# Kernel optimization log

Measured on AMD Instinct MI355X. Metric: run time of the kernel, lower is better.

## Reference

```python
import jax, jax.numpy as jnp
import numpy as np

D = 1024
H = 16
DK = D // H
SCALE = 1.0 / jnp.sqrt(jnp.float32(DK))


def setup_inputs() -> dict:
    key0 = jax.random.key(0)
    ks = jax.random.split(key0, 11)
    B, S = 2, 2048
    std = 1.0 / np.sqrt(D)
    inp = {
        "query": jax.random.normal(ks[0], (B, S, D), jnp.float32),
        "key": jax.random.normal(ks[1], (B, S, D), jnp.float32),
        "value": jax.random.normal(ks[2], (B, S, D), jnp.float32),
        "wq": jax.random.normal(ks[3], (D, D), jnp.float32) * std,
        "bq": jax.random.normal(ks[4], (D,), jnp.float32) * std,
        "wk": jax.random.normal(ks[5], (D, D), jnp.float32) * std,
        "bk": jax.random.normal(ks[6], (D,), jnp.float32) * std,
        "wv": jax.random.normal(ks[7], (D, D), jnp.float32) * std,
        "bv": jax.random.normal(ks[8], (D,), jnp.float32) * std,
        "wo": jax.random.normal(ks[9], (D, D), jnp.float32) * std,
        "bo": jax.random.normal(ks[10], (D,), jnp.float32) * std,
    }
    return inp


def _split_heads(x):
    # [B,S,D] -> [B,H,S,dk]
    B, S, _ = x.shape
    return x.reshape(B, S, H, DK).transpose(0, 2, 1, 3)


def reference(query, key, value, wq, bq, wk, bk, wv, bv, wo, bo):
    B, S, _ = query.shape
    # Linear projections (torch nn.Linear: x @ W^T + b)
    q = _split_heads(query @ wq.T + bq)
    k = _split_heads(key @ wk.T + bk)
    v = _split_heads(value @ wv.T + bv)
    # Scaled dot-product attention scores [B,H,S,S]
    scores = jnp.einsum("bhqd,bhkd->bhqk", q * SCALE, k)
    attention = jax.nn.softmax(scores, axis=-1)
    # Dropout in eval mode == identity
    out = jnp.einsum("bhqk,bhkd->bhqd", attention, v)
    out = out.transpose(0, 2, 1, 3).reshape(B, S, D)
    out = out @ wo.T + bo
    return out, attention
```

## Files before the change

### kernel.cpp

```cpp
#include <hip/hip_runtime.h>
#include <stdint.h>

typedef __attribute__((ext_vector_type(4))) float f32x4;
typedef __attribute__((ext_vector_type(8))) short short8;
typedef __attribute__((ext_vector_type(2))) unsigned int u32x2;

#define MFMA16(a, b, c) __builtin_amdgcn_mfma_f32_16x16x32_bf16((a), (b), (c), 0, 0, 0)

__device__ __forceinline__ unsigned short f2bf(float f) {
  unsigned int x = __float_as_uint(f);
  return (unsigned short)((x + 0x7fffu + ((x >> 16) & 1u)) >> 16);
}

__device__ __forceinline__ unsigned int cvtpk(float lo, float hi) {
  unsigned int d;
  asm("v_cvt_pk_bf16_f32 %0, %1, %2" : "=v"(d) : "v"(lo), "v"(hi));
  return d;
}

__device__ __forceinline__ void gl2lds16(const void* g, void* l) {
  __builtin_amdgcn_global_load_lds((const __attribute__((address_space(1))) void*)g,
                                   (__attribute__((address_space(3))) void*)l, 16, 0, 0);
}

__device__ __forceinline__ void load8cv(const float* __restrict__ s, void* d) {
  const f32x4* p = (const f32x4*)s;
  f32x4 a = p[0], b = p[1];
  short8 t;
  t[0] = (short)f2bf(a[0]); t[1] = (short)f2bf(a[1]);
  t[2] = (short)f2bf(a[2]); t[3] = (short)f2bf(a[3]);
  t[4] = (short)f2bf(b[0]); t[5] = (short)f2bf(b[1]);
  t[6] = (short)f2bf(b[2]); t[7] = (short)f2bf(b[3]);
  *(short8*)d = t;
}

#define BAR_V4 asm volatile("s_waitcnt vmcnt(4)\ns_barrier" ::: "memory")
#define BAR_V0 asm volatile("s_waitcnt vmcnt(0)\ns_barrier" ::: "memory")
#define BAR_RAW asm volatile("s_barrier" ::: "memory")

__global__ __launch_bounds__(256) void cast_weights(const float* __restrict__ wq,
                                                    const float* __restrict__ wk,
                                                    const float* __restrict__ wv,
                                                    const float* __restrict__ wo,
                                                    unsigned short* __restrict__ dst) {
  int i = blockIdx.x * 256 + threadIdx.x;
  int which = i >> 17;
  int off = (i & 131071) * 8;
  const float* src = which == 0 ? wq : which == 1 ? wk : which == 2 ? wv : wo;
  load8cv(src + off, dst + (size_t)which * 1048576 + off);
}

__global__ __launch_bounds__(256) void qkv_proj(const float* __restrict__ q_in,
                                                const float* __restrict__ k_in,
                                                const float* __restrict__ v_in,
                                                const unsigned short* __restrict__ W16,
                                                const float* __restrict__ bq,
                                                const float* __restrict__ bk,
                                                const float* __restrict__ bv,
                                                unsigned short* __restrict__ Q16,
                                                unsigned short* __restrict__ K16,
                                                unsigned short* __restrict__ V16) {
  const int z = blockIdx.z;
  const float* A = z == 0 ? q_in : z == 1 ? k_in : v_in;
  const unsigned short* Bt = W16 + (size_t)z * 1048576;
  const float* bias = z == 0 ? bq : z == 1 ? bk : bv;
  unsigned short* C = z == 0 ? Q16 : z == 1 ? K16 : V16;
  const float oscale = z == 0 ? 0.125f : 1.0f;
  const int K = 1024, N = 1024;

  __shared__ __align__(16) char lds[24576];
  char* As = lds;
  char* Bs = lds + 16384;
  const int tid = threadIdx.x;
  const int lane = tid & 63;
  const int wv = tid >> 6;
  const int g = lane >> 4, r = lane & 15;
  const int wm = wv >> 1, wn = wv & 1;
  const int m0 = blockIdx.y * 128, n0 = blockIdx.x * 64;

  f32x4 acc[4][2];
#pragma unroll
  for (int m = 0; m < 4; ++m)
#pragma unroll
    for (int n = 0; n < 2; ++n) acc[m][n] = (f32x4){0.f, 0.f, 0.f, 0.f};

  for (int k0 = 0; k0 < K; k0 += 64) {
    __syncthreads();
#pragma unroll
    for (int i = 0; i < 2; ++i) {
      int c = (wv * 2 + i) * 64 + lane;
      int row = c >> 3;
      gl2lds16(Bt + (size_t)(n0 + row) * K + k0 + (c & 7) * 8, Bs + (wv * 2 + i) * 1024);
    }
#pragma unroll
    for (int i = 0; i < 4; ++i) {
      int c = tid + i * 256;
      int row = c >> 3, e = (c & 7) * 8;
      load8cv(A + (size_t)(m0 + row) * K + k0 + e, As + c * 16);
    }
    __syncthreads();
#pragma unroll
    for (int kk = 0; kk < 2; ++kk) {
      short8 af[4], bfr[2];
#pragma unroll
      for (int m = 0; m < 4; ++m)
        af[m] = *(const short8*)(As + (wm * 64 + m * 16 + r) * 128 + kk * 64 + g * 16);
#pragma unroll
      for (int n = 0; n < 2; ++n)
        bfr[n] = *(const short8*)(Bs + (wn * 32 + n * 16 + r) * 128 + kk * 64 + g * 16);
#pragma unroll
      for (int m = 0; m < 4; ++m)
#pragma unroll
        for (int n = 0; n < 2; ++n) acc[m][n] = MFMA16(af[m], bfr[n], acc[m][n]);
    }
  }

#pragma unroll
  for (int n = 0; n < 2; ++n) {
    int col = n0 + wn * 32 + n * 16 + r;
    float bv_ = bias[col];
#pragma unroll
    for (int m = 0; m < 4; ++m)
#pragma unroll
      for (int i = 0; i < 4; ++i) {
        int rowg = m0 + wm * 64 + m * 16 + 4 * g + i;
        C[(size_t)rowg * N + col] = f2bf((acc[m][n][i] + bv_) * oscale);
      }
  }
}

__global__ __launch_bounds__(256) void o_proj(const unsigned short* __restrict__ A,
                                              const unsigned short* __restrict__ Bt,
                                              const float* __restrict__ bias,
                                              float* __restrict__ C) {
  const int K = 1024, N = 1024;
  __shared__ __align__(16) char lds[24576];
  char* As = lds;
  char* Bs = lds + 16384;
  const int tid = threadIdx.x;
  const int lane = tid & 63;
  const int wv = tid >> 6;
  const int g = lane >> 4, r = lane & 15;
  const int wm = wv >> 1, wn = wv & 1;
  const int m0 = blockIdx.y * 128, n0 = blockIdx.x * 64;

  f32x4 acc[4][2];
#pragma unroll
  for (int m = 0; m < 4; ++m)
#pragma unroll
    for (int n = 0; n < 2; ++n) acc[m][n] = (f32x4){0.f, 0.f, 0.f, 0.f};

  for (int k0 = 0; k0 < K; k0 += 64) {
    __syncthreads();
#pragma unroll
    for (int i = 0; i < 2; ++i) {
      int c = (wv * 2 + i) * 64 + lane;
      int row = c >> 3;
      gl2lds16(Bt + (size_t)(n0 + row) * K + k0 + (c & 7) * 8, Bs + (wv * 2 + i) * 1024);
    }
#pragma unroll
    for (int i = 0; i < 4; ++i) {
      int c = (wv * 4 + i) * 64 + lane;
      int row = c >> 3;
      gl2lds16(A + (size_t)(m0 + row) * K + k0 + (c & 7) * 8, As + (wv * 4 + i) * 1024);
    }
    __syncthreads();
#pragma unroll
    for (int kk = 0; kk < 2; ++kk) {
      short8 af[4], bfr[2];
#pragma unroll
      for (int m = 0; m < 4; ++m)
        af[m] = *(const short8*)(As + (wm * 64 + m * 16 + r) * 128 + kk * 64 + g * 16);
#pragma unroll
      for (int n = 0; n < 2; ++n)
        bfr[n] = *(const short8*)(Bs + (wn * 32 + n * 16 + r) * 128 + kk * 64 + g * 16);
#pragma unroll
      for (int m = 0; m < 4; ++m)
#pragma unroll
        for (int n = 0; n < 2; ++n) acc[m][n] = MFMA16(af[m], bfr[n], acc[m][n]);
    }
  }

#pragma unroll
  for (int n = 0; n < 2; ++n) {
    int col = n0 + wn * 32 + n * 16 + r;
    float bv_ = bias[col];
#pragma unroll
    for (int m = 0; m < 4; ++m)
#pragma unroll
      for (int i = 0; i < 4; ++i) {
        int rowg = m0 + wm * 64 + m * 16 + 4 * g + i;
        C[(size_t)rowg * N + col] = acc[m][n][i] + bv_;
      }
  }
}

__global__ __launch_bounds__(256) void transpose_v(const unsigned short* __restrict__ V,
                                                   unsigned short* __restrict__ Vt) {
  int t = blockIdx.x * 256 + threadIdx.x;
  int d = t & 63;
  int sc = (t >> 6) & 255;
  int bh = t >> 14;
  int b = bh >> 4, h = bh & 15;
  unsigned short vals[8];
#pragma unroll
  for (int j = 0; j < 8; ++j)
    vals[j] = V[(size_t)(b * 2048 + sc * 8 + j) * 1024 + h * 64 + d];
  *(short8*)&Vt[((size_t)bh * 64 + d) * 2048 + sc * 8] = *(short8*)vals;
}

__global__ __launch_bounds__(256, 4) void attn_fused(const unsigned short* __restrict__ Q,
                                                     const unsigned short* __restrict__ K,
                                                     const unsigned short* __restrict__ Vt,
                                                     float* __restrict__ attn,
                                                     unsigned short* __restrict__ O) {
  __shared__ __align__(16) char lds[40960];
  const int tid = threadIdx.x;
  const int lane = tid & 63;
  const int wv = tid >> 6;
  const int g = lane >> 4, r = lane & 15;
  int nb = (blockIdx.x & 7) * 128 + (blockIdx.x >> 3);
  const int qt = nb & 31, bh = nb >> 5, h = bh & 15, b = bh >> 4;
  const int qloc = qt * 64 + wv * 16;
  const int qrow0 = b * 2048 + qloc;
  const unsigned short* Kbh = K + (size_t)b * 2048 * 1024 + h * 64;
  const unsigned short* Vbh = Vt + (size_t)bh * 64 * 2048;
  float* attn_bh = attn + (size_t)bh * 2048 * 2048;
  char* pb = lds + 32768 + wv * 2048;
  const int swr = (r & 7) << 4;

  short8 qf[2];
#pragma unroll
  for (int kk = 0; kk < 2; ++kk)
    qf[kk] = *(const short8*)&Q[(size_t)(qrow0 + r) * 1024 + h * 64 + kk * 32 + g * 8];

#define P1_ISSUE(bb, ktt)                                                      \
  do {                                                                         \
    _Pragma("unroll") for (int i_ = 0; i_ < 4; ++i_) {                         \
      int c_ = (wv * 4 + i_) * 64 + lane;                                      \
      int kr_ = c_ >> 3;                                                       \
      int scb_ = ((c_ & 7) * 16) ^ ((kr_ & 7) << 4);                           \
      gl2lds16(Kbh + (size_t)((ktt) + kr_) * 1024 + (scb_ >> 1),               \
               (bb) + (wv * 4 + i_) * 1024);                                   \
    }                                                                          \
  } while (0)
#define P2_ISSUE(bb, ktt)                                                      \
  do {                                                                         \
    _Pragma("unroll") for (int i_ = 0; i_ < 4; ++i_) {                         \
      int c_ = (wv * 4 + i_) * 64 + lane;                                      \
      int kr_ = (c_ >> 3) & 63;                                                \
      int scb_ = ((c_ & 7) * 16) ^ ((kr_ & 7) << 4);                           \
      const unsigned short* src_ =                                             \
          (c_ < 512) ? (Kbh + (size_t)((ktt) + kr_) * 1024 + (scb_ >> 1))      \
                     : (Vbh + (size_t)kr_ * 2048 + (ktt) + (scb_ >> 1));       \
      gl2lds16(src_, (bb) + (wv * 4 + i_) * 1024);                             \
    }                                                                          \
  } while (0)

  float lrow = 0.f;
  int cur = 0;
  P1_ISSUE(lds, 0);
  for (int t = 0; t < 16; ++t) {
    char* bcur = lds + (cur << 14);
    char* bnxt = lds + ((cur ^ 1) << 14);
    if (t < 15) {
      P1_ISSUE(bnxt, (t + 1) * 128);
      BAR_V4;
    } else {
      BAR_V0;
    }
#pragma unroll
    for (int ct = 0; ct < 8; ++ct) {
      int row = ct * 16 + r;
      int sw = (row & 7) << 4;
      short8 kf0 = *(const short8*)(bcur + ((row * 128 + g * 16) ^ sw));
      short8 kf1 = *(const short8*)(bcur + ((row * 128 + 64 + g * 16) ^ sw));
      f32x4 s = (f32x4){0.f, 0.f, 0.f, 0.f};
      s = MFMA16(kf0, qf[0], s);
      s = MFMA16(kf1, qf[1], s);
      lrow += (__expf(s[0]) + __expf(s[1])) + (__expf(s[2]) + __expf(s[3]));
    }
    BAR_RAW;
    cur ^= 1;
  }
  {
    lrow += __shfl_xor(lrow, 16);
    lrow += __shfl_xor(lrow, 32);
  }
  const float negml = -__logf(lrow);
  const f32x4 cinit = (f32x4){negml, negml, negml, negml};

  f32x4 oacc[4];
#pragma unroll
  for (int i = 0; i < 4; ++i) oacc[i] = (f32x4){0.f, 0.f, 0.f, 0.f};

  float* arow = attn_bh + (size_t)(qloc + r) * 2048 + 4 * g;
  cur = 0;
  P2_ISSUE(lds, 0);
  for (int t = 0; t < 32; ++t) {
    char* bcur = lds + (cur << 14);
    char* bnxt = lds + ((cur ^ 1) << 14);
    int kt = t * 64;
    if (t < 31) {
      P2_ISSUE(bnxt, kt + 64);
      BAR_V4;
    } else {
      BAR_V0;
    }
#pragma unroll
    for (int ct = 0; ct < 4; ++ct) {
      int row = ct * 16 + r;
      int sw = (row & 7) << 4;
      short8 kf0 = *(const short8*)(bcur + ((row * 128 + g * 16) ^ sw));
      short8 kf1 = *(const short8*)(bcur + ((row * 128 + 64 + g * 16) ^ sw));
      f32x4 s = MFMA16(kf0, qf[0], cinit);
      s = MFMA16(kf1, qf[1], s);
      f32x4 p;
      p[0] = __expf(s[0]); p[1] = __expf(s[1]);
      p[2] = __expf(s[2]); p[3] = __expf(s[3]);
      *(f32x4*)(arow + kt + 16 * ct) = p;
      u32x2 pk;
      pk[0] = cvtpk(p[0], p[1]);
      pk[1] = cvtpk(p[2], p[3]);
      *(u32x2*)(pb + ((r * 128 + (ct * 16 + 4 * g) * 2) ^ swr)) = pk;
    }
#pragma unroll
    for (int kk2 = 0; kk2 < 2; ++kk2) {
      short8 pa = *(const short8*)(pb + ((r * 128 + kk2 * 64 + g * 16) ^ swr));
#pragma unroll
      for (int ct2 = 0; ct2 < 4; ++ct2) {
        int vrow = ct2 * 16 + r;
        short8 vf = *(const short8*)(bcur + 8192 +
                                     ((vrow * 128 + kk2 * 64 + g * 16) ^ ((vrow & 7) << 4)));
        oacc[ct2] = MFMA16(pa, vf, oacc[ct2]);
      }
    }
    BAR_RAW;
    cur ^= 1;
  }
#pragma unroll
  for (int ct2 = 0; ct2 < 4; ++ct2)
#pragma unroll
    for (int i = 0; i < 4; ++i)
      O[(size_t)(qrow0 + 4 * g + i) * 1024 + h * 64 + ct2 * 16 + r] = f2bf(oacc[ct2][i]);
#undef P1_ISSUE
#undef P2_ISSUE
}

extern "C" void kernel_launch(void* const* d_in, const int* in_sizes, int n_in,
                              void* d_out, int out_size, void* d_ws, size_t ws_size,
                              hipStream_t stream) {
  const float* q_in = (const float*)d_in[0];
  const float* k_in = (const float*)d_in[1];
  const float* v_in = (const float*)d_in[2];
  const float* wq = (const float*)d_in[3];
  const float* bq = (const float*)d_in[4];
  const float* wk = (const float*)d_in[5];
  const float* bk = (const float*)d_in[6];
  const float* wv = (const float*)d_in[7];
  const float* bv = (const float*)d_in[8];
  const float* wo = (const float*)d_in[9];
  const float* bo = (const float*)d_in[10];

  char* ws = (char*)d_ws;
  const size_t MB8 = 8ull * 1024 * 1024;
  unsigned short* W16 = (unsigned short*)(ws);
  unsigned short* Q16 = (unsigned short*)(ws + MB8);
  unsigned short* K16 = (unsigned short*)(ws + 2 * MB8);
  unsigned short* V16 = (unsigned short*)(ws + 3 * MB8);
  unsigned short* Vt  = (unsigned short*)(ws + 4 * MB8);
  unsigned short* O16 = (unsigned short*)(ws + 3 * MB8);

  float* out = (float*)d_out;
  float* attn = out + 4194304ull;

  dim3 blk(256);
  cast_weights<<<dim3(2048), blk, 0, stream>>>(wq, wk, wv, wo, W16);
  qkv_proj<<<dim3(16, 32, 3), blk, 0, stream>>>(q_in, k_in, v_in, W16, bq, bk, bv, Q16, K16, V16);
  transpose_v<<<dim3(2048), blk, 0, stream>>>(V16, Vt);
  attn_fused<<<dim3(1024), blk, 0, stream>>>(Q16, K16, Vt, attn, O16);
  o_proj<<<dim3(16, 32), blk, 0, stream>>>(O16, W16 + 3145728, bo, out);
}
```

Measured before the change: 321.2 us.

## Pre-cast activations to bf16 and load V fragments directly into registers

Result: slower. 328.6 us (+2.3%).

```diff
diff --git a/kernel.cpp b/kernel.cpp
--- a/kernel.cpp
+++ b/kernel.cpp
@@ -35,24 +35,40 @@
 }
 
 #define BAR_V4 asm volatile("s_waitcnt vmcnt(4)\ns_barrier" ::: "memory")
+#define BAR_V10 asm volatile("s_waitcnt vmcnt(10)\ns_barrier" ::: "memory")
 #define BAR_V0 asm volatile("s_waitcnt vmcnt(0)\ns_barrier" ::: "memory")
 #define BAR_RAW asm volatile("s_barrier" ::: "memory")
 
-__global__ __launch_bounds__(256) void cast_weights(const float* __restrict__ wq,
-                                                    const float* __restrict__ wk,
-                                                    const float* __restrict__ wv,
-                                                    const float* __restrict__ wo,
-                                                    unsigned short* __restrict__ dst) {
-  int i = blockIdx.x * 256 + threadIdx.x;
-  int which = i >> 17;
-  int off = (i & 131071) * 8;
-  const float* src = which == 0 ? wq : which == 1 ? wk : which == 2 ? wv : wo;
-  load8cv(src + off, dst + (size_t)which * 1048576 + off);
-}
-
-__global__ __launch_bounds__(256) void qkv_proj(const float* __restrict__ q_in,
+__global__ __launch_bounds__(256) void cast_all(const float* __restrict__ wq,
+                                                const float* __restrict__ wk,
+                                                const float* __restrict__ wv,
+                                                const float* __restrict__ wo,
+                                                const float* __restrict__ q_in,
                                                 const float* __restrict__ k_in,
                                                 const float* __restrict__ v_in,
+                                                unsigned short* __restrict__ W16,
+                                                unsigned short* __restrict__ Qin,
+                                                unsigned short* __restrict__ Kin,
+                                                unsigned short* __restrict__ Vin) {
+  int i = blockIdx.x * 256 + threadIdx.x;
+  if (i < 524288) {
+    int which = i >> 17;
+    int off = (i & 131071) * 8;
+    const float* src = which == 0 ? wq : which == 1 ? wk : which == 2 ? wv : wo;
+    load8cv(src + off, W16 + (size_t)which * 1048576 + off);
+  } else {
+    int j = i - 524288;
+    int which = j >> 19;
+    int off = (j & 524287) * 8;
+    const float* src = which == 0 ? q_in : which == 1 ? k_in : v_in;
+    unsigned short* dst = which == 0 ? Qin : which == 1 ? Kin : Vin;
+    load8cv(src + off, dst + off);
+  }
+}
+
+__global__ __launch_bounds__(256) void qkv_proj(const unsigned short* __restrict__ Qin,
+                                                const unsigned short* __restrict__ Kin,
+                                                const unsigned short* __restrict__ Vin,
                                                 const unsigned short* __restrict__ W16,
                                                 const float* __restrict__ bq,
                                                 const float* __restrict__ bk,
@@ -61,7 +77,7 @@
                                                 unsigned short* __restrict__ K16,
                                                 unsigned short* __restrict__ V16) {
   const int z = blockIdx.z;
-  const float* A = z == 0 ? q_in : z == 1 ? k_in : v_in;
+  const unsigned short* A = z == 0 ? Qin : z == 1 ? Kin : Vin;
   const unsigned short* Bt = W16 + (size_t)z * 1048576;
   const float* bias = z == 0 ? bq : z == 1 ? bk : bv;
   unsigned short* C = z == 0 ? Q16 : z == 1 ? K16 : V16;
@@ -94,9 +110,9 @@
     }
 #pragma unroll
     for (int i = 0; i < 4; ++i) {
-      int c = tid + i * 256;
-      int row = c >> 3, e = (c & 7) * 8;
-      load8cv(A + (size_t)(m0 + row) * K + k0 + e, As + c * 16);
+      int c = (wv * 4 + i) * 64 + lane;
+      int row = c >> 3;
+      gl2lds16(A + (size_t)(m0 + row) * K + k0 + (c & 7) * 8, As + (wv * 4 + i) * 1024);
     }
     __syncthreads();
 #pragma unroll
@@ -246,14 +262,12 @@
   } while (0)
 #define P2_ISSUE(bb, ktt)                                                      \
   do {                                                                         \
-    _Pragma("unroll") for (int i_ = 0; i_ < 4; ++i_) {                         \
-      int c_ = (wv * 4 + i_) * 64 + lane;                                      \
-      int kr_ = (c_ >> 3) & 63;                                                \
+    _Pragma("unroll") for (int i_ = 0; i_ < 2; ++i_) {                         \
+      int c_ = (wv * 2 + i_) * 64 + lane;                                      \
+      int kr_ = c_ >> 3;                                                       \
       int scb_ = ((c_ & 7) * 16) ^ ((kr_ & 7) << 4);                           \
-      const unsigned short* src_ =                                             \
-          (c_ < 512) ? (Kbh + (size_t)((ktt) + kr_) * 1024 + (scb_ >> 1))      \
-                     : (Vbh + (size_t)kr_ * 2048 + (ktt) + (scb_ >> 1));       \
-      gl2lds16(src_, (bb) + (wv * 4 + i_) * 1024);                             \
+      gl2lds16(Kbh + (size_t)((ktt) + kr_) * 1024 + (scb_ >> 1),               \
+               (bb) + (wv * 2 + i_) * 1024);                                   \
     }                                                                          \
   } while (0)
 
@@ -283,10 +297,8 @@
     BAR_RAW;
     cur ^= 1;
   }
-  {
-    lrow += __shfl_xor(lrow, 16);
-    lrow += __shfl_xor(lrow, 32);
-  }
+  lrow += __shfl_xor(lrow, 16);
+  lrow += __shfl_xor(lrow, 32);
   const float negml = -__logf(lrow);
   const f32x4 cinit = (f32x4){negml, negml, negml, negml};
 
@@ -295,18 +307,21 @@
   for (int i = 0; i < 4; ++i) oacc[i] = (f32x4){0.f, 0.f, 0.f, 0.f};
 
   float* arow = attn_bh + (size_t)(qloc + r) * 2048 + 4 * g;
+  const unsigned short* Vlane = Vbh + (size_t)r * 2048 + g * 8;
   cur = 0;
   P2_ISSUE(lds, 0);
   for (int t = 0; t < 32; ++t) {
     char* bcur = lds + (cur << 14);
     char* bnxt = lds + ((cur ^ 1) << 14);
     int kt = t * 64;
-    if (t < 31) {
-      P2_ISSUE(bnxt, kt + 64);
-      BAR_V4;
-    } else {
-      BAR_V0;
-    }
+    short8 vreg[2][4];
+#pragma unroll
+    for (int kk2 = 0; kk2 < 2; ++kk2)
+#pragma unroll
+      for (int c2 = 0; c2 < 4; ++c2)
+        vreg[kk2][c2] = *(const short8*)(Vlane + (size_t)(c2 * 16) * 2048 + kt + kk2 * 32);
+    if (t < 31) P2_ISSUE(bnxt, kt + 64);
+    BAR_V10;
 #pragma unroll
     for (int ct = 0; ct < 4; ++ct) {
       int row = ct * 16 + r;
@@ -324,17 +339,15 @@
       pk[1] = cvtpk(p[2], p[3]);
       *(u32x2*)(pb + ((r * 128 + (ct * 16 + 4 * g) * 2) ^ swr)) = pk;
     }
+    __builtin_amdgcn_s_setprio(1);
 #pragma unroll
     for (int kk2 = 0; kk2 < 2; ++kk2) {
       short8 pa = *(const short8*)(pb + ((r * 128 + kk2 * 64 + g * 16) ^ swr));
 #pragma unroll
-      for (int ct2 = 0; ct2 < 4; ++ct2) {
-        int vrow = ct2 * 16 + r;
-        short8 vf = *(const short8*)(bcur + 8192 +
-                                     ((vrow * 128 + kk2 * 64 + g * 16) ^ ((vrow & 7) << 4)));
-        oacc[ct2] = MFMA16(pa, vf, oacc[ct2]);
-      }
-    }
+      for (int ct2 = 0; ct2 < 4; ++ct2)
+        oacc[ct2] = MFMA16(pa, vreg[kk2][ct2], oacc[ct2]);
+    }
+    __builtin_amdgcn_s_setprio(0);
     BAR_RAW;
     cur ^= 1;
   }
@@ -364,19 +377,22 @@
 
   char* ws = (char*)d_ws;
   const size_t MB8 = 8ull * 1024 * 1024;
-  unsigned short* W16 = (unsigned short*)(ws);
-  unsigned short* Q16 = (unsigned short*)(ws + MB8);
-  unsigned short* K16 = (unsigned short*)(ws + 2 * MB8);
-  unsigned short* V16 = (unsigned short*)(ws + 3 * MB8);
-  unsigned short* Vt  = (unsigned short*)(ws + 4 * MB8);
-  unsigned short* O16 = (unsigned short*)(ws + 3 * MB8);
+  unsigned short* W16  = (unsigned short*)(ws);
+  unsigned short* Qin  = (unsigned short*)(ws + MB8);
+  unsigned short* Kin  = (unsigned short*)(ws + 2 * MB8);
+  unsigned short* Vin  = (unsigned short*)(ws + 3 * MB8);
+  unsigned short* Q16  = (unsigned short*)(ws + 4 * MB8);
+  unsigned short* K16  = (unsigned short*)(ws + 5 * MB8);
+  unsigned short* V16  = (unsigned short*)(ws + 6 * MB8);
+  unsigned short* Vt   = (unsigned short*)(ws + 7 * MB8);
+  unsigned short* O16  = (unsigned short*)(ws + 8 * MB8);
 
   float* out = (float*)d_out;
   float* attn = out + 4194304ull;
 
   dim3 blk(256);
-  cast_weights<<<dim3(2048), blk, 0, stream>>>(wq, wk, wv, wo, W16);
-  qkv_proj<<<dim3(16, 32, 3), blk, 0, stream>>>(q_in, k_in, v_in, W16, bq, bk, bv, Q16, K16, V16);
+  cast_all<<<dim3(8192), blk, 0, stream>>>(wq, wk, wv, wo, q_in, k_in, v_in, W16, Qin, Kin, Vin);
+  qkv_proj<<<dim3(16, 32, 3), blk, 0, stream>>>(Qin, Kin, Vin, W16, bq, bk, bv, Q16, K16, V16);
   transpose_v<<<dim3(2048), blk, 0, stream>>>(V16, Vt);
   attn_fused<<<dim3(1024), blk, 0, stream>>>(Q16, K16, Vt, attn, O16);
   o_proj<<<dim3(16, 32), blk, 0, stream>>>(O16, W16 + 3145728, bo, out);
```
